# Optimization experiments

Measured on AMD Instinct MI355X. Metric: run time of the kernel, lower is better.

Reference implementation:

```python
import jax, jax.numpy as jnp
import numpy as np


def setup_inputs() -> dict:
    key = jax.random.key(0)
    ks = jax.random.split(key, 6)
    B, H, KVH, D = 8, 32, 8, 128
    PAGES_PER_SEQ, PAGE_SIZE, L_MAX = 512, 16, 4096
    total_pages = B * PAGES_PER_SEQ  # 4096
    kv_len = PAGES_PER_SEQ * PAGE_SIZE  # 8192 tokens per sequence
    q = jax.random.normal(ks[0], (B, H, 1, D), dtype=jnp.float32)
    paged_kv_cache = jax.random.normal(ks[1], (total_pages, 2, KVH, PAGE_SIZE, D), dtype=jnp.float32)
    kv_page_indptr = (jnp.arange(B + 1, dtype=jnp.int32) * PAGES_PER_SEQ)
    kv_page_indices = jax.random.permutation(ks[2], total_pages).astype(jnp.int32)
    sparse_ind = jax.random.randint(ks[3], (B, H, L_MAX), 0, kv_len, dtype=jnp.int32)
    sparse_nnz = jax.random.randint(ks[4], (B, H), 1, L_MAX + 1, dtype=jnp.int32)
    return {
        "q": q,
        "paged_kv_cache": paged_kv_cache,
        "kv_page_indptr": kv_page_indptr,
        "kv_page_indices": kv_page_indices,
        "sparse_ind": sparse_ind,
        "sparse_nnz": sparse_nnz,
    }


def reference(q, paged_kv_cache, kv_page_indptr, kv_page_indices, sparse_ind, sparse_nnz):
    # q: [B, H, 1, D]; paged_kv_cache: [P, 2, KVH, PS, D]
    B, H, _, D = q.shape
    KVH, PS = paged_kv_cache.shape[2], paged_kv_cache.shape[3]
    groups = H // KVH
    L = sparse_ind.shape[-1]
    scale = jnp.float32(1.0 / (D ** 0.5))

    # Paged-table lookup: token index -> (logical page, offset) -> physical page id
    page_idx = sparse_ind // PS               # [B, H, L]
    off_in_page = sparse_ind % PS             # [B, H, L]
    page_id = kv_page_indices[kv_page_indptr[:B][:, None, None] + page_idx]  # [B, H, L]

    kv_head = (jnp.arange(H) // groups)[None, :, None]  # GQA head mapping, [1, H, 1]
    K = paged_kv_cache[page_id, 0, kv_head, off_in_page]  # [B, H, L, D]
    V = paged_kv_cache[page_id, 1, kv_head, off_in_page]  # [B, H, L, D]

    qk = jnp.einsum("bhd,bhld->bhl", q[:, :, 0, :], K)
    mask = jnp.arange(L)[None, None, :] < sparse_nnz[:, :, None]
    # Kernel uses additive -1e6 for masked lanes (K loaded as 0 -> qk==0)
    scores = jnp.where(mask, qk * scale, jnp.float32(-1e6))
    p = jax.nn.softmax(scores, axis=-1)       # online-softmax is math-equivalent
    out = jnp.einsum("bhl,bhld->bhd", p, V)
    return out[:, :, None, :]                  # [B, H, 1, D]
```

## Files before the change

kernel.cpp:

```cpp
#include <hip/hip_runtime.h>
#include <math.h>

#define BB   8
#define HH   32
#define KVHH 8
#define DD   128
#define PSZ  16
#define LMAX 4096
#define CHUNK 256
#define NCHUNK (LMAX / CHUNK)

#define PAGE_STRIDE (2 * KVHH * PSZ * DD)
#define KV_OFFSET   (KVHH * PSZ * DD)
#define HEAD_STRIDE (PSZ * DD)

__global__ __launch_bounds__(256) void attn_partial(
    const float* __restrict__ q,
    const float* __restrict__ cache,
    const int*   __restrict__ indptr,
    const int*   __restrict__ pageind,
    const int*   __restrict__ sind,
    const int*   __restrict__ snnz,
    float* __restrict__ ws_m,
    float* __restrict__ ws_l,
    float* __restrict__ ws_acc)
{
    const int blk   = blockIdx.x;
    const int xcd   = blk & 7;
    const int slot  = (blk >> 3) & 63;
    const int super = blk >> 9;
    const int g     = super * 8 + xcd;
    const int b     = g >> 3;
    const int kvh   = g & 7;
    const int h     = (kvh << 2) + (slot >> 4);
    const int chunk = slot & 15;
    const int bh    = b * HH + h;
    const int tid   = threadIdx.x;

    const int nnz  = snnz[bh];
    const int l0   = chunk * CHUNK;
    const int widx = bh * NCHUNK + chunk;

    if (l0 >= nnz) {
        if (tid == 0) { ws_m[widx] = -1e30f; ws_l[widx] = 0.0f; }
        if (tid < DD) ws_acc[widx * DD + tid] = 0.0f;
        return;
    }
    const int nrows = min(nnz - l0, CHUNK);
    const int nr64  = (nrows + 63) & ~63;
    const int nbat  = nr64 >> 6;

    __shared__ unsigned s_base[CHUNK];
    __shared__ float    s_p[CHUNK];
    __shared__ float    s_red[16];
    __shared__ float    s_acc[8][DD];

    const int indbase = indptr[b];
    const int* si = sind + bh * LMAX + l0;
    {
        unsigned base = 0u;
        if (tid < nrows) {
            const int idx = si[tid];
            const int pid = pageind[indbase + (idx >> 4)];
            base = (unsigned)pid * PAGE_STRIDE
                 + (unsigned)(kvh * HEAD_STRIDE + (idx & 15) * DD);
        }
        s_base[tid] = base;
    }
    __syncthreads();

    const int lane32 = tid & 31;
    const int hw     = tid >> 5;
    const float4 q4  = *(const float4*)(q + bh * DD + lane32 * 4);
    const float cscale = 0.08838834764831845f * 1.4426950408889634f;

    {
        float4 k[8];
        #pragma unroll
        for (int r = 0; r < 8; r++)
            k[r] = *(const float4*)(cache + s_base[hw + r * 8] + lane32 * 4);

        for (int t = 0; t < nbat; ++t) {
            const int i = hw + (t << 6);
            float4 kn[8];
            if (t + 1 < nbat) {
                #pragma unroll
                for (int r = 0; r < 8; r++)
                    kn[r] = *(const float4*)(cache + s_base[i + 64 + r * 8] + lane32 * 4);
            }
            float s[8];
            #pragma unroll
            for (int r = 0; r < 8; r++)
                s[r] = k[r].x*q4.x + k[r].y*q4.y + k[r].z*q4.z + k[r].w*q4.w;
            #pragma unroll
            for (int m = 16; m >= 1; m >>= 1) {
                #pragma unroll
                for (int r = 0; r < 8; r++) s[r] += __shfl_xor(s[r], m);
            }
            if (lane32 == 0) {
                #pragma unroll
                for (int r = 0; r < 8; r++)
                    s_p[i + r * 8] = (i + r * 8 < nrows) ? s[r] * cscale : -1e30f;
            }
            if (t + 1 < nbat) {
                #pragma unroll
                for (int r = 0; r < 8; r++) k[r] = kn[r];
            }
        }
    }

    float4 v[8];
    #pragma unroll
    for (int r = 0; r < 8; r++)
        v[r] = *(const float4*)(cache + s_base[hw + r * 8] + KV_OFFSET + lane32 * 4);

    __syncthreads();

    const float sc = (tid < nr64) ? s_p[tid] : -1e30f;
    float wm = sc;
    #pragma unroll
    for (int m = 32; m >= 1; m >>= 1) wm = fmaxf(wm, __shfl_xor(wm, m));
    const int wv = tid >> 6;
    if ((tid & 63) == 0) s_red[wv] = wm;
    __syncthreads();
    const float M = fmaxf(fmaxf(s_red[0], s_red[1]), fmaxf(s_red[2], s_red[3]));
    const float p = (tid < nr64) ? exp2f(sc - M) : 0.0f;
    if (tid < nr64) s_p[tid] = p;
    float wl = p;
    #pragma unroll
    for (int m = 32; m >= 1; m >>= 1) wl += __shfl_xor(wl, m);
    if ((tid & 63) == 0) s_red[8 + wv] = wl;
    __syncthreads();

    float4 acc = make_float4(0.f, 0.f, 0.f, 0.f);
    for (int t = 0; t < nbat; ++t) {
        const int i = hw + (t << 6);
        float4 vn[8];
        if (t + 1 < nbat) {
            #pragma unroll
            for (int r = 0; r < 8; r++)
                vn[r] = *(const float4*)(cache + s_base[i + 64 + r * 8] + KV_OFFSET + lane32 * 4);
        }
        #pragma unroll
        for (int r = 0; r < 8; r++) {
            const float pr = s_p[i + r * 8];
            acc.x += pr * v[r].x;
            acc.y += pr * v[r].y;
            acc.z += pr * v[r].z;
            acc.w += pr * v[r].w;
        }
        if (t + 1 < nbat) {
            #pragma unroll
            for (int r = 0; r < 8; r++) v[r] = vn[r];
        }
    }

    *(float4*)&s_acc[hw][lane32 * 4] = acc;
    __syncthreads();

    if (tid < DD) {
        float a = 0.f;
        #pragma unroll
        for (int i = 0; i < 8; i++) a += s_acc[i][tid];
        ws_acc[widx * DD + tid] = a;
        if (tid == 0) {
            ws_m[widx] = M;
            ws_l[widx] = s_red[8] + s_red[9] + s_red[10] + s_red[11];
        }
    }
}

__global__ __launch_bounds__(128) void attn_combine(
    const float* __restrict__ ws_m,
    const float* __restrict__ ws_l,
    const float* __restrict__ ws_acc,
    float* __restrict__ out)
{
    const int bh = blockIdx.x;
    const int d  = threadIdx.x;

    float M = -1e30f;
    #pragma unroll
    for (int i = 0; i < NCHUNK; i++) M = fmaxf(M, ws_m[bh * NCHUNK + i]);

    float tot = 0.f, a = 0.f;
    #pragma unroll
    for (int i = 0; i < NCHUNK; i++) {
        const float f = exp2f(ws_m[bh * NCHUNK + i] - M);
        tot += ws_l[bh * NCHUNK + i] * f;
        a   += ws_acc[(bh * NCHUNK + i) * DD + d] * f;
    }
    out[bh * DD + d] = a / tot;
}

extern "C" void kernel_launch(void* const* d_in, const int* in_sizes, int n_in,
                              void* d_out, int out_size, void* d_ws, size_t ws_size,
                              hipStream_t stream) {
    const float* q      = (const float*)d_in[0];
    const float* cache  = (const float*)d_in[1];
    const int*   indptr = (const int*)d_in[2];
    const int*   pgind  = (const int*)d_in[3];
    const int*   sind   = (const int*)d_in[4];
    const int*   snnz   = (const int*)d_in[5];
    float* out = (float*)d_out;

    float* ws_m   = (float*)d_ws;
    float* ws_l   = ws_m + BB * HH * NCHUNK;
    float* ws_acc = ws_l + BB * HH * NCHUNK;

    attn_partial<<<dim3(BB * HH * NCHUNK), dim3(256), 0, stream>>>(
        q, cache, indptr, pgind, sind, snnz, ws_m, ws_l, ws_acc);
    attn_combine<<<dim3(BB * HH), dim3(128), 0, stream>>>(
        ws_m, ws_l, ws_acc, out);
}
```

Measured before the change: 662.0 us.

## Stream KV pages once per GQA group using per-token sparse index histograms

Replaces the per-head gather of sparse KV rows with a histogram pass that counts, for each head, how often each KV position is selected. A new kernel then streams each page slice once per (batch, kv-head) group, computes scores for all four query heads sharing that KV head, weights exp2 scores by the counts, and skips rows no head uses. This cuts redundant and scattered loads of the same K/V rows across grouped heads. In exchange it adds zeroing and histogram kernels plus an 8 MB count buffer. It also drops the running-max subtraction, which risks overflow for large scores.

```diff
diff --git a/kernel.cpp b/kernel.cpp
--- a/kernel.cpp
+++ b/kernel.cpp
@@ -4,193 +4,213 @@
 #define BB   8
 #define HH   32
 #define KVHH 8
+#define GRP  4
 #define DD   128
 #define PSZ  16
 #define LMAX 4096
-#define CHUNK 256
-#define NCHUNK (LMAX / CHUNK)
+#define KVLEN 8192
+#define PPS  512
 
 #define PAGE_STRIDE (2 * KVHH * PSZ * DD)
 #define KV_OFFSET   (KVHH * PSZ * DD)
 #define HEAD_STRIDE (PSZ * DD)
 
-__global__ __launch_bounds__(256) void attn_partial(
-    const float* __restrict__ q,
-    const float* __restrict__ cache,
-    const int*   __restrict__ indptr,
-    const int*   __restrict__ pageind,
-    const int*   __restrict__ sind,
-    const int*   __restrict__ snnz,
-    float* __restrict__ ws_m,
+#define SLICES 32
+#define PGS    16
+#define ROWS   256
+
+#define CNT_WORDS (BB * HH * KVLEN)
+
+__global__ __launch_bounds__(256) void zero_cnt(uint4* __restrict__ cnt4) {
+    cnt4[blockIdx.x * 256 + threadIdx.x] = make_uint4(0u, 0u, 0u, 0u);
+}
+
+__global__ __launch_bounds__(256) void hist(
+    const int* __restrict__ sind,
+    const int* __restrict__ snnz,
+    unsigned*  __restrict__ cnt)
+{
+    const int bh  = blockIdx.x;
+    const int nnz = snnz[bh];
+    unsigned* c   = cnt + bh * KVLEN;
+    const int* si = sind + bh * LMAX;
+    for (int i = threadIdx.x; i < nnz; i += 256)
+        atomicAdd(&c[si[i]], 1u);
+}
+
+__global__ __launch_bounds__(256) void attn_stream(
+    const float*    __restrict__ q,
+    const float*    __restrict__ cache,
+    const int*      __restrict__ indptr,
+    const int*      __restrict__ pageind,
+    const unsigned* __restrict__ cnt,
     float* __restrict__ ws_l,
     float* __restrict__ ws_acc)
 {
     const int blk   = blockIdx.x;
-    const int xcd   = blk & 7;
-    const int slot  = (blk >> 3) & 63;
-    const int super = blk >> 9;
-    const int g     = super * 8 + xcd;
-    const int b     = g >> 3;
-    const int kvh   = g & 7;
-    const int h     = (kvh << 2) + (slot >> 4);
-    const int chunk = slot & 15;
-    const int bh    = b * HH + h;
+    const int slice = blk & 31;
+    const int grp   = blk >> 5;
+    const int b     = grp >> 3;
+    const int kvh   = grp & 7;
     const int tid   = threadIdx.x;
-
-    const int nnz  = snnz[bh];
-    const int l0   = chunk * CHUNK;
-    const int widx = bh * NCHUNK + chunk;
-
-    if (l0 >= nnz) {
-        if (tid == 0) { ws_m[widx] = -1e30f; ws_l[widx] = 0.0f; }
-        if (tid < DD) ws_acc[widx * DD + tid] = 0.0f;
-        return;
-    }
-    const int nrows = min(nnz - l0, CHUNK);
-    const int nr64  = (nrows + 63) & ~63;
-    const int nbat  = nr64 >> 6;
-
-    __shared__ unsigned s_base[CHUNK];
-    __shared__ float    s_p[CHUNK];
-    __shared__ float    s_red[16];
-    __shared__ float    s_acc[8][DD];
-
-    const int indbase = indptr[b];
-    const int* si = sind + bh * LMAX + l0;
-    {
-        unsigned base = 0u;
-        if (tid < nrows) {
-            const int idx = si[tid];
-            const int pid = pageind[indbase + (idx >> 4)];
-            base = (unsigned)pid * PAGE_STRIDE
-                 + (unsigned)(kvh * HEAD_STRIDE + (idx & 15) * DD);
-        }
-        s_base[tid] = base;
-    }
-    __syncthreads();
-
     const int lane32 = tid & 31;
     const int hw     = tid >> 5;
-    const float4 q4  = *(const float4*)(q + bh * DD + lane32 * 4);
+    const int bh0   = b * HH + kvh * GRP;
+
+    __shared__ int      s_pid[PGS];
+    __shared__ unsigned s_cnt[GRP][ROWS];
+    __shared__ float    s_pc[GRP][ROWS];
+    __shared__ float    s_acc[8][GRP][DD];
+    __shared__ float    s_lred[4][GRP];
+
+    if (tid < PGS) s_pid[tid] = pageind[indptr[b] + slice * PGS + tid];
+    {
+        const int r0 = slice * ROWS;
+        for (int i = tid; i < GRP * ROWS; i += 256) {
+            const int g = i >> 8, r = i & 255;
+            s_cnt[g][r] = cnt[(bh0 + g) * KVLEN + r0 + r];
+        }
+    }
+    __syncthreads();
+
+    const float4 q0 = *(const float4*)(q + (bh0 + 0) * DD + lane32 * 4);
+    const float4 q1 = *(const float4*)(q + (bh0 + 1) * DD + lane32 * 4);
+    const float4 q2 = *(const float4*)(q + (bh0 + 2) * DD + lane32 * 4);
+    const float4 q3 = *(const float4*)(q + (bh0 + 3) * DD + lane32 * 4);
     const float cscale = 0.08838834764831845f * 1.4426950408889634f;
 
+    for (int t = 0; t < PGS; ++t) {
+        const unsigned kbase = (unsigned)s_pid[t] * PAGE_STRIDE + kvh * HEAD_STRIDE;
+        const int rA = t * 16 + hw;
+        const int rB = rA + 8;
+        const unsigned cA0 = s_cnt[0][rA], cA1 = s_cnt[1][rA],
+                       cA2 = s_cnt[2][rA], cA3 = s_cnt[3][rA];
+        const unsigned cB0 = s_cnt[0][rB], cB1 = s_cnt[1][rB],
+                       cB2 = s_cnt[2][rB], cB3 = s_cnt[3][rB];
+        const bool fA = (cA0 | cA1 | cA2 | cA3) != 0u;
+        const bool fB = (cB0 | cB1 | cB2 | cB3) != 0u;
+
+        float sA0 = 0.f, sA1 = 0.f, sA2 = 0.f, sA3 = 0.f;
+        float sB0 = 0.f, sB1 = 0.f, sB2 = 0.f, sB3 = 0.f;
+        if (fA) {
+            const float4 k = *(const float4*)(cache + kbase + hw * DD + lane32 * 4);
+            sA0 = k.x*q0.x + k.y*q0.y + k.z*q0.z + k.w*q0.w;
+            sA1 = k.x*q1.x + k.y*q1.y + k.z*q1.z + k.w*q1.w;
+            sA2 = k.x*q2.x + k.y*q2.y + k.z*q2.z + k.w*q2.w;
+            sA3 = k.x*q3.x + k.y*q3.y + k.z*q3.z + k.w*q3.w;
+        }
+        if (fB) {
+            const float4 k = *(const float4*)(cache + kbase + (hw + 8) * DD + lane32 * 4);
+            sB0 = k.x*q0.x + k.y*q0.y + k.z*q0.z + k.w*q0.w;
+            sB1 = k.x*q1.x + k.y*q1.y + k.z*q1.z + k.w*q1.w;
+            sB2 = k.x*q2.x + k.y*q2.y + k.z*q2.z + k.w*q2.w;
+            sB3 = k.x*q3.x + k.y*q3.y + k.z*q3.z + k.w*q3.w;
+        }
+        #pragma unroll
+        for (int m = 16; m >= 1; m >>= 1) {
+            sA0 += __shfl_xor(sA0, m); sA1 += __shfl_xor(sA1, m);
+            sA2 += __shfl_xor(sA2, m); sA3 += __shfl_xor(sA3, m);
+            sB0 += __shfl_xor(sB0, m); sB1 += __shfl_xor(sB1, m);
+            sB2 += __shfl_xor(sB2, m); sB3 += __shfl_xor(sB3, m);
+        }
+        if (lane32 == 0) {
+            if (fA) {
+                s_pc[0][rA] = exp2f(sA0 * cscale) * (float)cA0;
+                s_pc[1][rA] = exp2f(sA1 * cscale) * (float)cA1;
+                s_pc[2][rA] = exp2f(sA2 * cscale) * (float)cA2;
+                s_pc[3][rA] = exp2f(sA3 * cscale) * (float)cA3;
+            } else {
+                s_pc[0][rA] = 0.f; s_pc[1][rA] = 0.f;
+                s_pc[2][rA] = 0.f; s_pc[3][rA] = 0.f;
+            }
+            if (fB) {
+                s_pc[0][rB] = exp2f(sB0 * cscale) * (float)cB0;
+                s_pc[1][rB] = exp2f(sB1 * cscale) * (float)cB1;
+                s_pc[2][rB] = exp2f(sB2 * cscale) * (float)cB2;
+                s_pc[3][rB] = exp2f(sB3 * cscale) * (float)cB3;
+            } else {
+                s_pc[0][rB] = 0.f; s_pc[1][rB] = 0.f;
+                s_pc[2][rB] = 0.f; s_pc[3][rB] = 0.f;
+            }
+        }
+    }
+    __syncthreads();
+
     {
-        float4 k[8];
+        float l0 = s_pc[0][tid], l1 = s_pc[1][tid],
+              l2 = s_pc[2][tid], l3 = s_pc[3][tid];
         #pragma unroll
-        for (int r = 0; r < 8; r++)
-            k[r] = *(const float4*)(cache + s_base[hw + r * 8] + lane32 * 4);
-
-        for (int t = 0; t < nbat; ++t) {
-            const int i = hw + (t << 6);
-            float4 kn[8];
-            if (t + 1 < nbat) {
-                #pragma unroll
-                for (int r = 0; r < 8; r++)
-                    kn[r] = *(const float4*)(cache + s_base[i + 64 + r * 8] + lane32 * 4);
-            }
-            float s[8];
-            #pragma unroll
-            for (int r = 0; r < 8; r++)
-                s[r] = k[r].x*q4.x + k[r].y*q4.y + k[r].z*q4.z + k[r].w*q4.w;
-            #pragma unroll
-            for (int m = 16; m >= 1; m >>= 1) {
-                #pragma unroll
-                for (int r = 0; r < 8; r++) s[r] += __shfl_xor(s[r], m);
-            }
-            if (lane32 == 0) {
-                #pragma unroll
-                for (int r = 0; r < 8; r++)
-                    s_p[i + r * 8] = (i + r * 8 < nrows) ? s[r] * cscale : -1e30f;
-            }
-            if (t + 1 < nbat) {
-                #pragma unroll
-                for (int r = 0; r < 8; r++) k[r] = kn[r];
-            }
-        }
-    }
-
-    float4 v[8];
-    #pragma unroll
-    for (int r = 0; r < 8; r++)
-        v[r] = *(const float4*)(cache + s_base[hw + r * 8] + KV_OFFSET + lane32 * 4);
-
-    __syncthreads();
-
-    const float sc = (tid < nr64) ? s_p[tid] : -1e30f;
-    float wm = sc;
-    #pragma unroll
-    for (int m = 32; m >= 1; m >>= 1) wm = fmaxf(wm, __shfl_xor(wm, m));
-    const int wv = tid >> 6;
-    if ((tid & 63) == 0) s_red[wv] = wm;
-    __syncthreads();
-    const float M = fmaxf(fmaxf(s_red[0], s_red[1]), fmaxf(s_red[2], s_red[3]));
-    const float p = (tid < nr64) ? exp2f(sc - M) : 0.0f;
-    if (tid < nr64) s_p[tid] = p;
-    float wl = p;
-    #pragma unroll
-    for (int m = 32; m >= 1; m >>= 1) wl += __shfl_xor(wl, m);
-    if ((tid & 63) == 0) s_red[8 + wv] = wl;
-    __syncthreads();
-
-    float4 acc = make_float4(0.f, 0.f, 0.f, 0.f);
-    for (int t = 0; t < nbat; ++t) {
-        const int i = hw + (t << 6);
-        float4 vn[8];
-        if (t + 1 < nbat) {
-            #pragma unroll
-            for (int r = 0; r < 8; r++)
-                vn[r] = *(const float4*)(cache + s_base[i + 64 + r * 8] + KV_OFFSET + lane32 * 4);
-        }
+        for (int m = 32; m >= 1; m >>= 1) {
+            l0 += __shfl_xor(l0, m); l1 += __shfl_xor(l1, m);
+            l2 += __shfl_xor(l2, m); l3 += __shfl_xor(l3, m);
+        }
+        const int wv = tid >> 6;
+        if ((tid & 63) == 0) {
+            s_lred[wv][0] = l0; s_lred[wv][1] = l1;
+            s_lred[wv][2] = l2; s_lred[wv][3] = l3;
+        }
+    }
+    __syncthreads();
+    if (tid < GRP) {
+        ws_l[(bh0 + tid) * SLICES + slice] =
+            s_lred[0][tid] + s_lred[1][tid] + s_lred[2][tid] + s_lred[3][tid];
+    }
+
+    float4 a0 = make_float4(0.f,0.f,0.f,0.f), a1 = a0, a2 = a0, a3 = a0;
+    for (int t = 0; t < PGS; ++t) {
+        const unsigned vbase = (unsigned)s_pid[t] * PAGE_STRIDE + KV_OFFSET
+                             + kvh * HEAD_STRIDE;
+        const int rA = t * 16 + hw;
+        const int rB = rA + 8;
+        const float pA0 = s_pc[0][rA], pA1 = s_pc[1][rA],
+                    pA2 = s_pc[2][rA], pA3 = s_pc[3][rA];
+        const float pB0 = s_pc[0][rB], pB1 = s_pc[1][rB],
+                    pB2 = s_pc[2][rB], pB3 = s_pc[3][rB];
+        if (pA0 != 0.f || pA1 != 0.f || pA2 != 0.f || pA3 != 0.f) {
+            const float4 v = *(const float4*)(cache + vbase + hw * DD + lane32 * 4);
+            a0.x += pA0*v.x; a0.y += pA0*v.y; a0.z += pA0*v.z; a0.w += pA0*v.w;
+            a1.x += pA1*v.x; a1.y += pA1*v.y; a1.z += pA1*v.z; a1.w += pA1*v.w;
+            a2.x += pA2*v.x; a2.y += pA2*v.y; a2.z += pA2*v.z; a2.w += pA2*v.w;
+            a3.x += pA3*v.x; a3.y += pA3*v.y; a3.z += pA3*v.z; a3.w += pA3*v.w;
+        }
+        if (pB0 != 0.f || pB1 != 0.f || pB2 != 0.f || pB3 != 0.f) {
+            const float4 v = *(const float4*)(cache + vbase + (hw + 8) * DD + lane32 * 4);
+            a0.x += pB0*v.x; a0.y += pB0*v.y; a0.z += pB0*v.z; a0.w += pB0*v.w;
+            a1.x += pB1*v.x; a1.y += pB1*v.y; a1.z += pB1*v.z; a1.w += pB1*v.w;
+            a2.x += pB2*v.x; a2.y += pB2*v.y; a2.z += pB2*v.z; a2.w += pB2*v.w;
+            a3.x += pB3*v.x; a3.y += pB3*v.y; a3.z += pB3*v.z; a3.w += pB3*v.w;
+        }
+    }
+
+    *(float4*)&s_acc[hw][0][lane32 * 4] = a0;
+    *(float4*)&s_acc[hw][1][lane32 * 4] = a1;
+    *(float4*)&s_acc[hw][2][lane32 * 4] = a2;
+    *(float4*)&s_acc[hw][3][lane32 * 4] = a3;
+    __syncthreads();
+
+    for (int pair = tid; pair < GRP * DD; pair += 256) {
+        const int g = pair >> 7, d = pair & 127;
+        float s = 0.f;
         #pragma unroll
-        for (int r = 0; r < 8; r++) {
-            const float pr = s_p[i + r * 8];
-            acc.x += pr * v[r].x;
-            acc.y += pr * v[r].y;
-            acc.z += pr * v[r].z;
-            acc.w += pr * v[r].w;
-        }
-        if (t + 1 < nbat) {
-            #pragma unroll
-            for (int r = 0; r < 8; r++) v[r] = vn[r];
-        }
-    }
-
-    *(float4*)&s_acc[hw][lane32 * 4] = acc;
-    __syncthreads();
-
-    if (tid < DD) {
-        float a = 0.f;
-        #pragma unroll
-        for (int i = 0; i < 8; i++) a += s_acc[i][tid];
-        ws_acc[widx * DD + tid] = a;
-        if (tid == 0) {
-            ws_m[widx] = M;
-            ws_l[widx] = s_red[8] + s_red[9] + s_red[10] + s_red[11];
-        }
+        for (int w = 0; w < 8; w++) s += s_acc[w][g][d];
+        ws_acc[((bh0 + g) * SLICES + slice) * DD + d] = s;
     }
 }
 
 __global__ __launch_bounds__(128) void attn_combine(
-    const float* __restrict__ ws_m,
     const float* __restrict__ ws_l,
     const float* __restrict__ ws_acc,
     float* __restrict__ out)
 {
     const int bh = blockIdx.x;
     const int d  = threadIdx.x;
-
-    float M = -1e30f;
+    float l = 0.f, a = 0.f;
     #pragma unroll
-    for (int i = 0; i < NCHUNK; i++) M = fmaxf(M, ws_m[bh * NCHUNK + i]);
-
-    float tot = 0.f, a = 0.f;
-    #pragma unroll
-    for (int i = 0; i < NCHUNK; i++) {
-        const float f = exp2f(ws_m[bh * NCHUNK + i] - M);
-        tot += ws_l[bh * NCHUNK + i] * f;
-        a   += ws_acc[(bh * NCHUNK + i) * DD + d] * f;
-    }
-    out[bh * DD + d] = a / tot;
+    for (int s = 0; s < SLICES; s++) {
+        l += ws_l[bh * SLICES + s];
+        a += ws_acc[(bh * SLICES + s) * DD + d];
+    }
+    out[bh * DD + d] = a / l;
 }
 
 extern "C" void kernel_launch(void* const* d_in, const int* in_sizes, int n_in,
@@ -204,12 +224,13 @@
     const int*   snnz   = (const int*)d_in[5];
     float* out = (float*)d_out;
 
-    float* ws_m   = (float*)d_ws;
-    float* ws_l   = ws_m + BB * HH * NCHUNK;
-    float* ws_acc = ws_l + BB * HH * NCHUNK;
-
-    attn_partial<<<dim3(BB * HH * NCHUNK), dim3(256), 0, stream>>>(
-        q, cache, indptr, pgind, sind, snnz, ws_m, ws_l, ws_acc);
-    attn_combine<<<dim3(BB * HH), dim3(128), 0, stream>>>(
-        ws_m, ws_l, ws_acc, out);
-}
+    unsigned* cnt   = (unsigned*)d_ws;
+    float*    ws_l  = (float*)((char*)d_ws + (size_t)CNT_WORDS * 4);
+    float*    ws_acc = ws_l + BB * HH * SLICES;
+
+    zero_cnt<<<dim3(CNT_WORDS / 4 / 256), dim3(256), 0, stream>>>((uint4*)d_ws);
+    hist<<<dim3(BB * HH), dim3(256), 0, stream>>>(sind, snnz, cnt);
+    attn_stream<<<dim3(64 * SLICES), dim3(256), 0, stream>>>(
+        q, cache, indptr, pgind, cnt, ws_l, ws_acc);
+    attn_combine<<<dim3(BB * HH), dim3(128), 0, stream>>>(ws_l, ws_acc, out);
+}
```

Measured after the change: 711.6 us. 7.5% more time.
